# Kernel tuning notes

Hardware: AMD Instinct MI355X
Metric: run time of the kernel (lower is better)

Reference implementation:

```python
import jax, jax.numpy as jnp
from jax import lax
import numpy as np

DIM = 768        # d_model (mamba-130m)
D_IN = 1024      # vision encoder feature dim
NQ = 384         # num_queries
NB = 12          # num_blocks
BATCH = 2
LSEQ = 1024      # image tokens
DI = 2 * DIM     # mamba d_inner (expand=2)
DS = 16          # d_state
DC = 4           # d_conv
DTR = 48         # dt_rank = ceil(768/16)
NH = 16          # attention heads
HD = DIM // NH
NM = NB + 2      # mamba instances: fwd-enc, bwd-enc, one per block


def _ln(x, g, b):
    m = jnp.mean(x, -1, keepdims=True)
    v = jnp.mean((x - m) ** 2, -1, keepdims=True)
    return (x - m) * lax.rsqrt(v + 1e-5) * g + b


def _mamba(x, in_w, conv_w, conv_b, xproj_w, dt_w, dt_b, A_log, Dp, out_w):
    # x: (B, L, DIM)
    Bb = x.shape[0]
    xz = x @ in_w.T                      # (B, L, 2*DI)
    xi, z = jnp.split(xz, 2, -1)
    # depthwise causal conv1d over time
    xc = lax.conv_general_dilated(xi.transpose(0, 2, 1), conv_w[:, None, :], (1,),
                                  [(DC - 1, 0)], feature_group_count=DI,
                                  dimension_numbers=('NCH', 'OIH', 'NCH'))
    xc = jax.nn.silu((xc + conv_b[None, :, None]).transpose(0, 2, 1))  # (B, L, DI)
    dbl = xc @ xproj_w.T                 # (B, L, DTR + 2*DS)
    dt, Bm, Cm = jnp.split(dbl, [DTR, DTR + DS], -1)
    dt = jax.nn.softplus(dt @ dt_w.T + dt_b)   # (B, L, DI)
    A = -jnp.exp(A_log)                        # (DI, DS)
    dA = jnp.exp(dt[..., None] * A)            # (B, L, DI, DS)
    dBx = dt[..., None] * Bm[:, :, None, :] * xc[..., None]

    def step(h, inp):
        dA_t, dBx_t, C_t = inp
        h = dA_t * h + dBx_t
        return h, jnp.einsum('bds,bs->bd', h, C_t)

    h0 = jnp.zeros((Bb, DI, DS), x.dtype)
    _, ys = lax.scan(step, h0, (dA.transpose(1, 0, 2, 3), dBx.transpose(1, 0, 2, 3), Cm.transpose(1, 0, 2)))
    y = ys.transpose(1, 0, 2) + Dp * xc
    y = y * jax.nn.silu(z)
    return y @ out_w.T


def _local_allowed(nq, nk):
    # matches Attention.get_local_mask: query i attends to its contiguous key block
    kpq, extra = nk // nq, nk % nq
    i = jnp.arange(nq)
    start = i * kpq + jnp.minimum(i, extra)
    end = start + kpq + (i < extra)
    k = jnp.arange(nk)
    return (k[None, :] >= start[:, None]) & (k[None, :] < end[:, None])


def _mha(q_in, kv, in_w, in_b, out_w, out_b, allowed):
    # nn.MultiheadAttention(dim, 16, batch_first=True) cross-attention
    wq, wk, wv = jnp.split(in_w, 3, 0)
    bq, bk, bv = jnp.split(in_b, 3, 0)
    Bb = q_in.shape[0]
    q = (q_in @ wq.T + bq).reshape(Bb, -1, NH, HD)
    k = (kv @ wk.T + bk).reshape(Bb, -1, NH, HD)
    v = (kv @ wv.T + bv).reshape(Bb, -1, NH, HD)
    s = jnp.einsum('bqhd,bkhd->bhqk', q, k) / np.float32(np.sqrt(HD))
    s = jnp.where(allowed[None, None], s, -jnp.inf)
    a = jax.nn.softmax(s, -1)
    o = jnp.einsum('bhqk,bkhd->bqhd', a, v).reshape(Bb, -1, DIM)
    return o @ out_w.T + out_b


def _model(img_emb, queries, vision_proj_w, vision_proj_b, ln_vision_g, ln_vision_b,
           mamba_in_w, mamba_conv_w, mamba_conv_b, mamba_xproj_w, mamba_dt_w, mamba_dt_b,
           mamba_A_log, mamba_D, mamba_out_w, seq_norm_g, seq_norm_b,
           attn_in_w, attn_in_b, attn_out_w, attn_out_b, cross_w, cross_b):
    mp = lambda i: (mamba_in_w[i], mamba_conv_w[i], mamba_conv_b[i], mamba_xproj_w[i],
                    mamba_dt_w[i], mamba_dt_b[i], mamba_A_log[i], mamba_D[i], mamba_out_w[i])
    feats = _ln(img_emb @ vision_proj_w.T + vision_proj_b, ln_vision_g, ln_vision_b)
    fwd = _mamba(feats, *mp(0))
    bwd = jnp.flip(_mamba(jnp.flip(feats, 1), *mp(1)), 1)
    c = fwd + bwd + feats
    x = jnp.broadcast_to(queries, (img_emb.shape[0], NQ, DIM))
    allowed = _local_allowed(NQ, c.shape[1])
    for l in range(NB):
        x = _ln(x, seq_norm_g[l], seq_norm_b[l])
        x = _mamba(x, *mp(l + 2)) + x
        score = _mha(x, c, attn_in_w[l], attn_in_b[l], attn_out_w[l], attn_out_b[l], allowed)
        x = jnp.concatenate([x, score], -1) @ cross_w[l].T + cross_b[l]
    return x


_model_jit = jax.jit(_model)


def setup_inputs() -> dict:
    key = jax.random.key(0)
    ks = iter(jax.random.split(key, 24))
    rn = lambda shape, s=0.02: jax.random.normal(next(ks), shape, jnp.float32) * s
    A_log = jnp.broadcast_to(jnp.log(jnp.arange(1, DS + 1, dtype=jnp.float32)), (NM, DI, DS))
    return {
        'img_emb': rn((BATCH, LSEQ, D_IN), 1.0),
        'queries': rn((1, NQ, DIM)),
        'vision_proj_w': rn((DIM, D_IN)),
        'vision_proj_b': jnp.zeros((DIM,), jnp.float32),
        'ln_vision_g': jnp.ones((DIM,), jnp.float32),
        'ln_vision_b': jnp.zeros((DIM,), jnp.float32),
        'mamba_in_w': rn((NM, 2 * DI, DIM)),
        'mamba_conv_w': rn((NM, DI, DC), 0.1),
        'mamba_conv_b': jnp.zeros((NM, DI), jnp.float32),
        'mamba_xproj_w': rn((NM, DTR + 2 * DS, DI)),
        'mamba_dt_w': rn((NM, DI, DTR), 0.1),
        'mamba_dt_b': rn((NM, DI), 0.5),
        'mamba_A_log': A_log,
        'mamba_D': jnp.ones((NM, DI), jnp.float32),
        'mamba_out_w': rn((NM, DIM, DI)),
        'seq_norm_g': jnp.ones((NB, DIM), jnp.float32),
        'seq_norm_b': jnp.zeros((NB, DIM), jnp.float32),
        'attn_in_w': rn((NB, 3 * DIM, DIM)),
        'attn_in_b': jnp.zeros((NB, 3 * DIM), jnp.float32),
        'attn_out_w': rn((NB, DIM, DIM)),
        'attn_out_b': jnp.zeros((NB, DIM), jnp.float32),
        'cross_w': rn((NB, DIM, 2 * DIM)),
        'cross_b': jnp.zeros((NB, DIM), jnp.float32),
    }


def reference(img_emb, queries, vision_proj_w, vision_proj_b, ln_vision_g, ln_vision_b,
              mamba_in_w, mamba_conv_w, mamba_conv_b, mamba_xproj_w, mamba_dt_w, mamba_dt_b,
              mamba_A_log, mamba_D, mamba_out_w, seq_norm_g, seq_norm_b,
              attn_in_w, attn_in_b, attn_out_w, attn_out_b, cross_w, cross_b):
    return _model_jit(img_emb, queries, vision_proj_w, vision_proj_b, ln_vision_g, ln_vision_b,
                      mamba_in_w, mamba_conv_w, mamba_conv_b, mamba_xproj_w, mamba_dt_w, mamba_dt_b,
                      mamba_A_log, mamba_D, mamba_out_w, seq_norm_g, seq_norm_b,
                      attn_in_w, attn_in_b, attn_out_w, attn_out_b, cross_w, cross_b)
```

## Files before the change

kernel.cpp:

```cpp
#include <hip/hip_runtime.h>
#include <hip/hip_bf16.h>

#define DIMQ 768
#define D_IN 1024
#define NQ 384
#define NBK 12
#define BATCH 2
#define LSEQ 1024
#define DI 1536
#define DS 16
#define DTR 48
#define NH 16
#define HD 48

typedef __attribute__((ext_vector_type(8))) short short8;
typedef __attribute__((ext_vector_type(4))) float f32x4;

#define GF_BIAS 1
#define GF_SOFTPLUS 2
#define EPI_BIAS 1
#define EPI_ADDT 2

#define LOG2E 1.4426950408889634f

__device__ __forceinline__ unsigned short f2bf(float f) {
    unsigned int u = __builtin_bit_cast(unsigned int, f);
    u = (u + 0x7FFFu + ((u >> 16) & 1u)) >> 16;
    return (unsigned short)u;
}
__device__ __forceinline__ float bf2f(unsigned short h) {
    unsigned int u = ((unsigned int)h) << 16;
    return __builtin_bit_cast(float, u);
}

__device__ __forceinline__ void gload_lds16(const void* g, void* l) {
    __builtin_amdgcn_global_load_lds(
        (const __attribute__((address_space(1))) void*)g,
        (__attribute__((address_space(3))) void*)l, 16, 0, 0);
}

struct WTab {
    const float* src[10];
    long long dstOff[10];
    long long ps[10];
    int cum[10];
    int rows[10], cols[10], dcols[10];
    int n;
    int total;
};

__global__ void wconv_kernel(unsigned short* __restrict__ dst, WTab T)
{
    const int i = blockIdx.x * 256 + threadIdx.x;
    if (i >= T.total) return;
    int sI = 0;
    while (i >= T.cum[sI]) ++sI;
    const int e = i - (sI ? T.cum[sI - 1] : 0);
    const int dcols = T.dcols[sI];
    const int r = e / dcols;
    const int c = e - r * dcols;
    float v = 0.f;
    if (r < T.rows[sI] && c < T.cols[sI]) v = T.src[sI][(long long)r * T.cols[sI] + c];
    const unsigned short h = f2bf(v);
    const unsigned short l = f2bf(v - bf2f(h));
    dst[T.dstOff[sI] + e] = h;
    dst[T.dstOff[sI] + T.ps[sI] + e] = l;
}

struct LTab {
    const float* src[7];
    long long srcStride[7], dstOff[7], ps[7];
    int rows[7], cols[7], dcols[7], cum[7];
};

__global__ __launch_bounds__(256)
void wconv_layers(unsigned short* __restrict__ dst, long long layerStride, int lBase, LTab T)
{
    const int e = blockIdx.x * 256 + threadIdx.x;
    const int l = blockIdx.y + lBase;
    int sI = 0;
    while (e >= T.cum[sI]) ++sI;
    const int eo = e - (sI ? T.cum[sI - 1] : 0);
    const int dc = T.dcols[sI];
    const int r = eo / dc;
    const int c = eo - r * dc;
    float v = 0.f;
    if (r < T.rows[sI] && c < T.cols[sI])
        v = T.src[sI][(long long)l * T.srcStride[sI] + (long long)r * T.cols[sI] + c];
    const unsigned short h = f2bf(v);
    const unsigned short lo2 = f2bf(v - bf2f(h));
    unsigned short* d = dst + (long long)blockIdx.y * layerStride + T.dstOff[sI];
    d[eo] = h;
    d[T.ps[sI] + eo] = lo2;
}

__global__ __launch_bounds__(256, 3)
void gemm_direct(const float* __restrict__ Ag, const unsigned short* __restrict__ Bhl,
                 float* __restrict__ Cg, const float* __restrict__ biasg,
                 int M, int N, int K, int lda, int ldb, int ldc,
                 long long sA, long long sB, long long sC, long long sBias,
                 long long planeB, int flags)
{
    __shared__ __align__(16) unsigned short As[2][2][64][32];
    __shared__ __align__(16) unsigned short Bs[2][2][128][32];

    const int z = blockIdx.z;
    const float* A = Ag + (size_t)z * sA;
    const unsigned short* Bhi = Bhl + (size_t)z * sB;
    const unsigned short* Blo = Bhi + planeB;
    float* C = Cg + (size_t)z * sC;

    const int mBase = blockIdx.x * 64;
    const int nBase = blockIdx.y * 128;
    const int tid = threadIdx.x, lane = tid & 63, wave = tid >> 6;
    const int lm = lane & 15, lq = lane >> 4;
    const int wn = wave * 32;
    const int arow = tid >> 2, aq = tid & 3;
    const int brow = lane >> 2;
    const int bcol = ((lane & 3) ^ ((lane >> 3) & 3)) * 8;
    const int aunit = (aq ^ ((arow >> 1) & 3)) * 8;
    const int funit = (lq ^ ((lm >> 1) & 3)) * 8;

    const int ktiles = (K + 31) >> 5;

    auto issueB = [&](int t, int buf) {
#pragma unroll
        for (int cc = 0; cc < 4; ++cc) {
            const int chunk = wave * 4 + cc;
            const int pl = chunk >> 3;
            const int r16 = chunk & 7;
            const unsigned short* bp = pl ? Blo : Bhi;
            const int n = nBase + r16 * 16 + brow;
            gload_lds16(bp + (size_t)n * ldb + t * 32 + bcol, &Bs[buf][pl][r16 * 16][0]);
        }
    };
    auto loadA = [&](int t, float* v) {
        const int col = t * 32 + aq * 8;
        const float* src = A + (size_t)(mBase + arow) * lda + col;
#pragma unroll
        for (int u = 0; u < 2; ++u) {
            float4 t4 = make_float4(0.f, 0.f, 0.f, 0.f);
            if (col + u * 4 < K) t4 = *(const float4*)(src + u * 4);
            v[u*4+0]=t4.x; v[u*4+1]=t4.y; v[u*4+2]=t4.z; v[u*4+3]=t4.w;
        }
    };
    auto writeA = [&](const float* v, int buf) {
        short8 ph, plv;
#pragma unroll
        for (int j = 0; j < 8; ++j) {
            unsigned short h = f2bf(v[j]);
            ph[j] = (short)h;
            plv[j] = (short)f2bf(v[j] - bf2f(h));
        }
        *(short8*)&As[buf][0][arow][aunit] = ph;
        *(short8*)&As[buf][1][arow][aunit] = plv;
    };

    float av[8];
    issueB(0, 0);
    loadA(0, av);
    writeA(av, 0);

    f32x4 acc[4][2] = {};
    for (int t = 0; t < ktiles; ++t) {
        const int buf = t & 1;
        __syncthreads();
        const bool more = (t + 1) < ktiles;
        if (more) { issueB(t + 1, buf ^ 1); loadA(t + 1, av); }
        short8 ah[4], al[4], bh[2], bl[2];
#pragma unroll
        for (int i = 0; i < 4; ++i) {
            ah[i] = *(const short8*)&As[buf][0][16*i + lm][funit];
            al[i] = *(const short8*)&As[buf][1][16*i + lm][funit];
        }
#pragma unroll
        for (int j = 0; j < 2; ++j) {
            bh[j] = *(const short8*)&Bs[buf][0][wn + 16*j + lm][funit];
            bl[j] = *(const short8*)&Bs[buf][1][wn + 16*j + lm][funit];
        }
#pragma unroll
        for (int i = 0; i < 4; ++i)
#pragma unroll
            for (int j = 0; j < 2; ++j) {
                acc[i][j] = __builtin_amdgcn_mfma_f32_16x16x32_bf16(ah[i], bh[j], acc[i][j], 0, 0, 0);
                acc[i][j] = __builtin_amdgcn_mfma_f32_16x16x32_bf16(ah[i], bl[j], acc[i][j], 0, 0, 0);
                acc[i][j] = __builtin_amdgcn_mfma_f32_16x16x32_bf16(al[i], bh[j], acc[i][j], 0, 0, 0);
            }
        if (more) writeA(av, buf ^ 1);
    }

#pragma unroll
    for (int i = 0; i < 4; ++i)
#pragma unroll
        for (int j = 0; j < 2; ++j)
#pragma unroll
            for (int r = 0; r < 4; ++r) {
                const int m = mBase + i*16 + lq*4 + r;
                const int n = nBase + wn + j*16 + lm;
                float v = acc[i][j][r];
                if (flags & GF_BIAS)     v += biasg[(size_t)z * sBias + n];
                if (flags & GF_SOFTPLUS) v = (v > 20.f) ? v : log1pf(expf(v));
                C[(size_t)m * ldc + n] = v;
            }
}

__global__ __launch_bounds__(256, 3)
void gemm_splitk(const float* __restrict__ Ag, const unsigned short* __restrict__ Bhl,
                 float* __restrict__ Cp,
                 int M, int kLen, int S, int lda, int ldb, int ldP,
                 long long sA, long long sB, long long planeB)
{
    __shared__ __align__(16) unsigned short As[2][2][64][32];
    __shared__ __align__(16) unsigned short Bs[2][2][128][32];

    const int bz = blockIdx.z;
    const int s = bz % S, z = bz / S;
    const int kOff = s * kLen;
    const float* A = Ag + (size_t)z * sA;
    const unsigned short* Bhi = Bhl + (size_t)z * sB;
    const unsigned short* Blo = Bhi + planeB;

    const int mBase = blockIdx.x * 64;
    const int nBase = blockIdx.y * 128;
    const int tid = threadIdx.x, lane = tid & 63, wave = tid >> 6;
    const int lm = lane & 15, lq = lane >> 4;
    const int wn = wave * 32;
    const int arow = tid >> 2, aq = tid & 3;
    const int brow = lane >> 2;
    const int bcol = ((lane & 3) ^ ((lane >> 3) & 3)) * 8;
    const int aunit = (aq ^ ((arow >> 1) & 3)) * 8;
    const int funit = (lq ^ ((lm >> 1) & 3)) * 8;

    const int ktiles = kLen >> 5;

    auto issueB = [&](int t, int buf) {
#pragma unroll
        for (int cc = 0; cc < 4; ++cc) {
            const int chunk = wave * 4 + cc;
            const int pl = chunk >> 3;
            const int r16 = chunk & 7;
            const unsigned short* bp = pl ? Blo : Bhi;
            const int n = nBase + r16 * 16 + brow;
            gload_lds16(bp + (size_t)n * ldb + kOff + t * 32 + bcol, &Bs[buf][pl][r16 * 16][0]);
        }
    };
    auto loadA = [&](int t, float* v) {
        const float* src = A + (size_t)(mBase + arow) * lda + kOff + t * 32 + aq * 8;
#pragma unroll
        for (int u = 0; u < 2; ++u) {
            const float4 t4 = *(const float4*)(src + u * 4);
            v[u*4+0]=t4.x; v[u*4+1]=t4.y; v[u*4+2]=t4.z; v[u*4+3]=t4.w;
        }
    };
    auto writeA = [&](const float* v, int buf) {
        short8 ph, plv;
#pragma unroll
        for (int j = 0; j < 8; ++j) {
            unsigned short h = f2bf(v[j]);
            ph[j] = (short)h;
            plv[j] = (short)f2bf(v[j] - bf2f(h));
        }
        *(short8*)&As[buf][0][arow][aunit] = ph;
        *(short8*)&As[buf][1][arow][aunit] = plv;
    };

    float av[8];
    issueB(0, 0);
    loadA(0, av);
    writeA(av, 0);

    f32x4 acc[4][2] = {};
    for (int t = 0; t < ktiles; ++t) {
        const int buf = t & 1;
        __syncthreads();
        const bool more = (t + 1) < ktiles;
        if (more) { issueB(t + 1, buf ^ 1); loadA(t + 1, av); }
        short8 ah[4], al[4], bh[2], bl[2];
#pragma unroll
        for (int i = 0; i < 4; ++i) {
            ah[i] = *(const short8*)&As[buf][0][16*i + lm][funit];
            al[i] = *(const short8*)&As[buf][1][16*i + lm][funit];
        }
#pragma unroll
        for (int j = 0; j < 2; ++j) {
            bh[j] = *(const short8*)&Bs[buf][0][wn + 16*j + lm][funit];
            bl[j] = *(const short8*)&Bs[buf][1][wn + 16*j + lm][funit];
        }
#pragma unroll
        for (int i = 0; i < 4; ++i)
#pragma unroll
            for (int j = 0; j < 2; ++j) {
                acc[i][j] = __builtin_amdgcn_mfma_f32_16x16x32_bf16(ah[i], bh[j], acc[i][j], 0, 0, 0);
                acc[i][j] = __builtin_amdgcn_mfma_f32_16x16x32_bf16(ah[i], bl[j], acc[i][j], 0, 0, 0);
                acc[i][j] = __builtin_amdgcn_mfma_f32_16x16x32_bf16(al[i], bh[j], acc[i][j], 0, 0, 0);
            }
        if (more) writeA(av, buf ^ 1);
    }

    float* Cb = Cp + (size_t)bz * M * ldP;
#pragma unroll
    for (int i = 0; i < 4; ++i)
#pragma unroll
        for (int j = 0; j < 2; ++j)
#pragma unroll
            for (int r = 0; r < 4; ++r) {
                const int m = mBase + i*16 + lq*4 + r;
                const int n = nBase + wn + j*16 + lm;
                Cb[(size_t)m * ldP + n] = acc[i][j][r];
            }
}

__global__ void epi_kernel(const float* __restrict__ Cp, float* __restrict__ outF,
                           const float* __restrict__ bias, const float* __restrict__ addT,
                           int Z, int S, int M, int N, int ldP, int ldOut,
                           long long sOutZ, long long sBiasZ, int ldAdd, int flags)
{
    const int n4 = N >> 2;
    const int idx = blockIdx.x * 256 + threadIdx.x;
    if (idx >= Z * M * n4) return;
    const int c4 = idx % n4;
    const int rem = idx / n4;
    const int m = rem % M;
    const int z = rem / M;
    const int n = c4 * 4;
    const float* base = Cp + ((size_t)z * S * M + m) * ldP + n;
    float4 v = *(const float4*)base;
    for (int s = 1; s < S; ++s) {
        const float4 u = *(const float4*)(base + (size_t)s * M * ldP);
        v.x += u.x; v.y += u.y; v.z += u.z; v.w += u.w;
    }
    if (flags & EPI_BIAS) {
        const float4 b4 = *(const float4*)(bias + (size_t)z * sBiasZ + n);
        v.x += b4.x; v.y += b4.y; v.z += b4.z; v.w += b4.w;
    }
    if (flags & EPI_ADDT) {
        const float4 a4 = *(const float4*)(addT + (size_t)m * ldAdd + n);
        v.x += a4.x; v.y += a4.y; v.z += a4.z; v.w += a4.w;
    }
    *(float4*)(outF + (size_t)z * sOutZ + (size_t)m * ldOut + n) = v;
}

__global__ __launch_bounds__(256)
void epi_ln_kernel(const float* __restrict__ Cp, float* __restrict__ outF,
                   const float* __restrict__ bias,
                   const float* __restrict__ g, const float* __restrict__ b,
                   int S, int M, int ldP)
{
    const int m = blockIdx.x;
    const int tid = threadIdx.x;
    __shared__ float red[8];
    float v[3];
    float s = 0.f, s2 = 0.f;
#pragma unroll
    for (int j = 0; j < 3; ++j) {
        const int n = tid + j * 256;
        const float* pp = Cp + (size_t)m * ldP + n;
        float x = pp[0];
        for (int q = 1; q < S; ++q) x += pp[(size_t)q * M * ldP];
        x += bias[n];
        v[j] = x; s += x; s2 += x * x;
    }
#pragma unroll
    for (int o = 32; o; o >>= 1) { s += __shfl_xor(s, o); s2 += __shfl_xor(s2, o); }
    const int wv = tid >> 6;
    if ((tid & 63) == 0) { red[wv] = s; red[4 + wv] = s2; }
    __syncthreads();
    s  = red[0] + red[1] + red[2] + red[3];
    s2 = red[4] + red[5] + red[6] + red[7];
    const float mean = s * (1.f/768.f);
    const float var  = s2 * (1.f/768.f) - mean * mean;
    const float inv  = rsqrtf(var + 1e-5f);
#pragma unroll
    for (int j = 0; j < 3; ++j) {
        const int n = tid + j * 256;
        outF[(size_t)m * DIMQ + n] = (v[j] - mean) * inv * g[n] + b[n];
    }
}

__global__ void ln_kernel(const float* __restrict__ in, float* __restrict__ out,
                          const float* __restrict__ g, const float* __restrict__ b,
                          int rows, int srcMod)
{
    const int row = blockIdx.x * 4 + (threadIdx.x >> 6);
    const int lane = threadIdx.x & 63;
    if (row >= rows) return;
    const float* p = in + (size_t)(row % srcMod) * DIMQ;
    float v[12], s = 0.f, s2 = 0.f;
#pragma unroll
    for (int j = 0; j < 12; ++j) {
        v[j] = p[j*64 + lane];
        s += v[j];
        s2 += v[j]*v[j];
    }
#pragma unroll
    for (int o = 32; o; o >>= 1) { s += __shfl_xor(s, o); s2 += __shfl_xor(s2, o); }
    const float mean = s * (1.f/768.f);
    const float var  = s2 * (1.f/768.f) - mean*mean;
    const float inv  = rsqrtf(var + 1e-5f);
    float* q = out + (size_t)row * DIMQ;
#pragma unroll
    for (int j = 0; j < 12; ++j) {
        const int c = j*64 + lane;
        q[c] = (v[j] - mean) * inv * g[c] + b[c];
    }
}

__global__ void conv_kernel(const float* __restrict__ xz, float* __restrict__ xc,
                            const float* __restrict__ cw, const float* __restrict__ cb,
                            int Bn, int L, int instShift)
{
    const int idx = blockIdx.x * 256 + threadIdx.x;
    const int total = Bn * L * (DI/4);
    if (idx >= total) return;
    const int d4 = idx % (DI/4);
    const int t  = (idx / (DI/4)) % L;
    const int b  = idx / (L * (DI/4));
    const int inst = b >> instShift;
    const int d = d4 * 4;
    const float* base = xz + (size_t)(b * L) * 3072 + d;
    const float4 w0 = *(const float4*)(cw + (size_t)(inst*DI + d + 0) * 4);
    const float4 w1 = *(const float4*)(cw + (size_t)(inst*DI + d + 1) * 4);
    const float4 w2 = *(const float4*)(cw + (size_t)(inst*DI + d + 2) * 4);
    const float4 w3 = *(const float4*)(cw + (size_t)(inst*DI + d + 3) * 4);
    float4 acc = *(const float4*)(cb + (size_t)inst*DI + d);
    float4 xv[4];
#pragma unroll
    for (int j = 0; j < 4; ++j) {
        const int tt = t - 3 + j;
        xv[j] = (tt >= 0) ? *(const float4*)(base + (size_t)tt * 3072) : make_float4(0,0,0,0);
    }
    acc.x += xv[0].x*w0.x + xv[1].x*w0.y + xv[2].x*w0.z + xv[3].x*w0.w;
    acc.y += xv[0].y*w1.x + xv[1].y*w1.y + xv[2].y*w1.z + xv[3].y*w1.w;
    acc.z += xv[0].z*w2.x + xv[1].z*w2.y + xv[2].z*w2.z + xv[3].z*w2.w;
    acc.w += xv[0].w*w3.x + xv[1].w*w3.y + xv[2].w*w3.z + xv[3].w*w3.w;
    float4 o;
    o.x = acc.x / (1.f + expf(-acc.x));
    o.y = acc.y / (1.f + expf(-acc.y));
    o.z = acc.z / (1.f + expf(-acc.z));
    o.w = acc.w / (1.f + expf(-acc.w));
    *(float4*)(xc + (size_t)(b * L + t) * DI + d) = o;
}

__global__ __launch_bounds__(256)
void scan_p1(const float* __restrict__ dt, const float* __restrict__ dbl,
             const float* __restrict__ xc, const float* __restrict__ A_log,
             float* __restrict__ hend, float* __restrict__ sumdt,
             int L, int CL, int Bn, int instShift)
{
    const int d = blockIdx.x * 256 + threadIdx.x;
    const int b = blockIdx.y;
    const int c = blockIdx.z;
    const int inst = b >> instShift;
    const float* ap = A_log + ((size_t)inst * DI + d) * DS;
    float A2[16];
#pragma unroll
    for (int s = 0; s < 16; ++s) A2[s] = -expf(ap[s]) * LOG2E;
    float h[16] = {};
    float sd = 0.f;
    const int t0 = c * CL;
    const size_t rowbase = (size_t)b * L;
    for (int t = t0; t < t0 + CL; ++t) {
        const size_t row = rowbase + t;
        const float dtv = dt[row * DI + d];
        const float xcv = xc[row * DI + d];
        float Bv[16];
        *(float4*)(Bv + 0)  = *(const float4*)(dbl + row * 80 + 48);
        *(float4*)(Bv + 4)  = *(const float4*)(dbl + row * 80 + 52);
        *(float4*)(Bv + 8)  = *(const float4*)(dbl + row * 80 + 56);
        *(float4*)(Bv + 12) = *(const float4*)(dbl + row * 80 + 60);
        sd += dtv;
        const float bx = dtv * xcv;
#pragma unroll
        for (int s = 0; s < 16; ++s)
            h[s] = exp2f(dtv * A2[s]) * h[s] + bx * Bv[s];
    }
    float* hp = hend + (((size_t)c * Bn + b) * DI + d) * DS;
#pragma unroll
    for (int s = 0; s < 16; s += 4)
        *(float4*)(hp + s) = make_float4(h[s], h[s+1], h[s+2], h[s+3]);
    sumdt[((size_t)c * Bn + b) * DI + d] = sd;
}

__global__ void scan_p2(const float* __restrict__ hend, const float* __restrict__ sumdt,
                        const float* __restrict__ A_log, float* __restrict__ hstart,
                        int NC, int Bn, int instShift)
{
    const int gid = blockIdx.x * 256 + threadIdx.x;
    const int s = gid & 15;
    const int rem = gid >> 4;
    const int d = rem % DI;
    const int b = rem / DI;
    const int inst = b >> instShift;
    const float A2 = -expf(A_log[((size_t)inst * DI + d) * DS + s]) * LOG2E;
    float carry = 0.f;
    for (int c = 0; c < NC; ++c) {
        const size_t off = (((size_t)c * Bn + b) * DI + d) * DS + s;
        hstart[off] = carry;
        carry = exp2f(A2 * sumdt[((size_t)c * Bn + b) * DI + d]) * carry + hend[off];
    }
}

__global__ __launch_bounds__(256)
void scan_p3(const float* __restrict__ dt, const float* __restrict__ dbl,
             const float* __restrict__ xc, const float* __restrict__ xz,
             const float* __restrict__ A_log, const float* __restrict__ Dp,
             const float* __restrict__ hstart, float* __restrict__ y,
             int L, int CL, int Bn, int instShift)
{
    const int d = blockIdx.x * 256 + threadIdx.x;
    const int b = blockIdx.y;
    const int c = blockIdx.z;
    const int inst = b >> instShift;
    const float* ap = A_log + ((size_t)inst * DI + d) * DS;
    float A2[16];
#pragma unroll
    for (int s = 0; s < 16; ++s) A2[s] = -expf(ap[s]) * LOG2E;
    const float Dd = Dp[(size_t)inst * DI + d];
    float h[16];
    const float* hp = hstart + (((size_t)c * Bn + b) * DI + d) * DS;
#pragma unroll
    for (int s = 0; s < 16; s += 4) {
        const float4 t4 = *(const float4*)(hp + s);
        h[s] = t4.x; h[s+1] = t4.y; h[s+2] = t4.z; h[s+3] = t4.w;
    }
    const int t0 = c * CL;
    const size_t rowbase = (size_t)b * L;
    for (int t = t0; t < t0 + CL; ++t) {
        const size_t row = rowbase + t;
        const float dtv = dt[row * DI + d];
        const float xcv = xc[row * DI + d];
        const float zv  = xz[row * 3072 + DI + d];
        float Bv[16], Cv[16];
        *(float4*)(Bv + 0)  = *(const float4*)(dbl + row * 80 + 48);
        *(float4*)(Bv + 4)  = *(const float4*)(dbl + row * 80 + 52);
        *(float4*)(Bv + 8)  = *(const float4*)(dbl + row * 80 + 56);
        *(float4*)(Bv + 12) = *(const float4*)(dbl + row * 80 + 60);
        *(float4*)(Cv + 0)  = *(const float4*)(dbl + row * 80 + 64);
        *(float4*)(Cv + 4)  = *(const float4*)(dbl + row * 80 + 68);
        *(float4*)(Cv + 8)  = *(const float4*)(dbl + row * 80 + 72);
        *(float4*)(Cv + 12) = *(const float4*)(dbl + row * 80 + 76);
        const float bx = dtv * xcv;
#pragma unroll
        for (int s = 0; s < 16; ++s)
            h[s] = exp2f(dtv * A2[s]) * h[s] + bx * Bv[s];
        float p0 = 0.f, p1 = 0.f, p2 = 0.f, p3 = 0.f;
#pragma unroll
        for (int s = 0; s < 4; ++s) {
            p0 += h[s]      * Cv[s];
            p1 += h[s + 4]  * Cv[s + 4];
            p2 += h[s + 8]  * Cv[s + 8];
            p3 += h[s + 12] * Cv[s + 12];
        }
        const float p = (p0 + p1) + (p2 + p3);
        y[row * DI + d] = (p + Dd * xcv) * (zv / (1.f + expf(-zv)));
    }
}

__global__ void attn_kernel(const float* __restrict__ qP, const float* __restrict__ qBias,
                            const float* __restrict__ kv, float* __restrict__ o,
                            int S, int ldP)
{
    const int bi = blockIdx.x;
    const int b = bi / NQ, i = bi % NQ;
    const int tid = threadIdx.x;
    const int h = tid >> 2, r = tid & 3;
    int start, len;
    if (i < 256) { start = 3*i; len = 3; } else { start = 2*i + 256; len = 2; }
    const int col0 = h*48 + r*12;
    float qv[12];
#pragma unroll
    for (int u = 0; u < 12; ++u) {
        const int n = col0 + u;
        float x = qP[(size_t)bi * ldP + n];
        for (int s = 1; s < S; ++s) x += qP[((size_t)s * 768 + bi) * ldP + n];
        qv[u] = x + qBias[n];
    }
    float s[3] = {-1e30f, -1e30f, -1e30f};
    for (int j = 0; j < len; ++j) {
        const float* kp = kv + (size_t)(b*LSEQ + start + j) * 1536 + col0;
        float p = 0.f;
#pragma unroll
        for (int u = 0; u < 12; ++u) p += qv[u] * kp[u];
        p += __shfl_xor(p, 1);
        p += __shfl_xor(p, 2);
        s[j] = p * 0.14433756729740644f;
    }
    const float mx = fmaxf(s[0], fmaxf(s[1], s[2]));
    float e[3];
    e[0] = expf(s[0]-mx); e[1] = expf(s[1]-mx); e[2] = expf(s[2]-mx);
    const float inv = 1.f / (e[0] + e[1] + e[2]);
    float ov[12] = {};
    for (int j = 0; j < len; ++j) {
        const float w = e[j] * inv;
        const float* vp = kv + (size_t)(b*LSEQ + start + j) * 1536 + 768 + col0;
#pragma unroll
        for (int u = 0; u < 12; ++u) ov[u] += w * vp[u];
    }
    float* op = o + (size_t)bi * DIMQ + col0;
#pragma unroll
    for (int u = 0; u < 12; ++u) op[u] = ov[u];
}

__global__ void flip_kernel(float* __restrict__ X2)
{
    const int idx = blockIdx.x * 256 + threadIdx.x;
    if (idx >= 2*1024*192) return;
    const int d4 = idx % 192;
    const int t  = (idx / 192) % 1024;
    const int b  = idx / (192 * 1024);
    const size_t dst = ((size_t)((2+b)*1024 + t)) * DIMQ + d4*4;
    const size_t src = ((size_t)(b*1024 + (1023 - t))) * DIMQ + d4*4;
    *(float4*)(X2 + dst) = *(const float4*)(X2 + src);
}

__global__ void combine_kernel(const float* __restrict__ oe, const float* __restrict__ feats,
                               float* __restrict__ c)
{
    const int idx = blockIdx.x * 256 + threadIdx.x;
    if (idx >= 2*1024*192) return;
    const int d4 = idx % 192;
    const int t  = (idx / 192) % 1024;
    const int b  = idx / (192 * 1024);
    const size_t fw = ((size_t)(b*1024 + t)) * DIMQ + d4*4;
    const size_t bw = ((size_t)((2+b)*1024 + (1023 - t))) * DIMQ + d4*4;
    const float4 a = *(const float4*)(oe + fw);
    const float4 bb = *(const float4*)(oe + bw);
    const float4 f = *(const float4*)(feats + fw);
    float4 o;
    o.x = a.x + bb.x + f.x; o.y = a.y + bb.y + f.y;
    o.z = a.z + bb.z + f.z; o.w = a.w + bb.w + f.w;
    *(float4*)(c + fw) = o;
}

extern "C" void kernel_launch(void* const* d_in, const int* in_sizes, int n_in,
                              void* d_out, int out_size, void* d_ws, size_t ws_size,
                              hipStream_t stream) {
    const float* img_emb  = (const float*)d_in[0];
    const float* queries  = (const float*)d_in[1];
    const float* vis_w    = (const float*)d_in[2];
    const float* vis_b    = (const float*)d_in[3];
    const float* lnv_g    = (const float*)d_in[4];
    const float* lnv_b    = (const float*)d_in[5];
    const float* m_in_w   = (const float*)d_in[6];
    const float* m_conv_w = (const float*)d_in[7];
    const float* m_conv_b = (const float*)d_in[8];
    const float* m_xp_w   = (const float*)d_in[9];
    const float* m_dt_w   = (const float*)d_in[10];
    const float* m_dt_b   = (const float*)d_in[11];
    const float* m_A_log  = (const float*)d_in[12];
    const float* m_D      = (const float*)d_in[13];
    const float* m_out_w  = (const float*)d_in[14];
    const float* sn_g     = (const float*)d_in[15];
    const float* sn_b     = (const float*)d_in[16];
    const float* a_in_w   = (const float*)d_in[17];
    const float* a_in_b   = (const float*)d_in[18];
    const float* a_out_w  = (const float*)d_in[19];
    const float* a_out_b  = (const float*)d_in[20];
    const float* cr_w     = (const float*)d_in[21];
    const float* cr_b     = (const float*)d_in[22];
    float* out = (float*)d_out;

    float* ws = (float*)d_ws;
    auto alloc = [&](size_t n) { float* p = ws; ws += n; return p; };
    float* X2   = alloc((size_t)4096*768);
    float* xzb  = alloc((size_t)4096*3072);
    float* xcb  = alloc((size_t)4096*1536);
    float* dblb = alloc((size_t)4096*80);
    float* dtb  = alloc((size_t)4096*1536);
    float* yb   = alloc((size_t)4096*1536);
    float* oe   = alloc((size_t)4096*768);
    float* cbuf = alloc((size_t)2048*768);
    float* xn   = alloc((size_t)768*768);
    float* x1s  = alloc((size_t)768*1536);
    float* ob   = alloc((size_t)768*768);
    float* Cp   = alloc((size_t)2359296);
    unsigned short* wenc = (unsigned short*)alloc((size_t)16908288/2);

    const long long LAYER_USH = 14745600;
    const size_t usedFloats = (size_t)(ws - (float*)d_ws);
    const size_t needFull = (usedFloats + (size_t)12 * (LAYER_USH/2)) * 4;
    const bool bigW = ws_size >= needFull;
    unsigned short* wlayAll = (unsigned short*)ws;

    const size_t kvFloats = (size_t)12 * 2048 * 1536;
    const size_t needKV = needFull + kvFloats * 4;
    const bool kvHoist = bigW && ws_size >= needKV;
    float* kvAll = (float*)(wlayAll + (size_t)12 * LAYER_USH);

    const long long P_VIS = 768LL*1024;
    const long long P_IN  = 3072LL*768;
    const long long P_XP  = 128LL*1536;
    const long long P_DT  = 1536LL*64;
    const long long P_OUT = 768LL*1536;
    const long long P_AIN = 2304LL*768;
    const long long P_AOUT= 768LL*768;
    const long long P_CR  = 768LL*1536;
    const long long off_vis   = 0;
    const long long off_encIn = 2*P_VIS;
    const long long off_encXp = off_encIn + 4*P_IN;
    const long long off_encDt = off_encXp + 4*P_XP;
    const long long off_encOut= off_encDt + 4*P_DT;
    const long long off_in  = 0;
    const long long off_xp  = 2*P_IN;
    const long long off_dt  = off_xp + 2*P_XP;
    const long long off_out = off_dt + 2*P_DT;
    const long long off_aIn = off_out + 2*P_OUT;
    const long long off_aOut= off_aIn + 2*P_AIN;
    const long long off_cr  = off_aOut + 2*P_AOUT;

    auto addSeg = [](WTab& T, const float* src, int rows, int cols, int drows, int dcols,
                     long long dstOff) {
        const int k = T.n;
        T.src[k] = src; T.rows[k] = rows; T.cols[k] = cols; T.dcols[k] = dcols;
        T.ps[k] = (long long)drows * dcols;
        T.dstOff[k] = dstOff;
        T.total += drows * dcols;
        T.cum[k] = T.total;
        T.n = k + 1;
    };

    auto GD = [&](const float* A, const unsigned short* Bhl, long long planeB,
                  float* C, const float* bias,
                  int M, int N, int K, int lda, int ldb, int ldc,
                  long long sA, long long sB, long long sC, long long sBias,
                  int Z, int flags) {
        dim3 grid(M/64, N/128, Z);
        gemm_direct<<<grid, 256, 0, stream>>>(A, Bhl, C, bias, M, N, K, lda, ldb, ldc,
                                              sA, sB, sC, sBias, planeB, flags);
    };
    auto GS = [&](const float* A, const unsigned short* Bhl, long long planeB,
                  int M, int Ntile, int kLen, int S, int lda, int ldb, int ldP,
                  long long sA, long long sB, int Z) {
        dim3 grid(M/64, Ntile/128, Z*S);
        gemm_splitk<<<grid, 256, 0, stream>>>(A, Bhl, Cp, M, kLen, S, lda, ldb, ldP,
                                              sA, sB, planeB);
    };
    auto EPI = [&](float* outF, const float* bias, const float* addT,
                   int Z, int S, int M, int N, int ldP, int ldOut,
                   long long sOutZ, long long sBiasZ, int ldAdd, int flags) {
        const int total = Z * M * (N/4);
        epi_kernel<<<(total+255)/256, 256, 0, stream>>>(Cp, outF, bias, addT, Z, S, M, N,
                                                        ldP, ldOut, sOutZ, sBiasZ, ldAdd, flags);
    };

    {
        WTab T = {}; T.n = 0; T.total = 0;
        addSeg(T, vis_w, 768, 1024, 768, 1024, off_vis);
        addSeg(T, m_in_w,               3072, 768, 3072, 768, off_encIn);
        addSeg(T, m_in_w + 3072*768,    3072, 768, 3072, 768, off_encIn + 2*P_IN);
        addSeg(T, m_xp_w,               80, 1536, 128, 1536, off_encXp);
        addSeg(T, m_xp_w + 80*1536,     80, 1536, 128, 1536, off_encXp + 2*P_XP);
        addSeg(T, m_dt_w,               1536, 48, 1536, 64, off_encDt);
        addSeg(T, m_dt_w + 1536*48,     1536, 48, 1536, 64, off_encDt + 2*P_DT);
        addSeg(T, m_out_w,              768, 1536, 768, 1536, off_encOut);
        addSeg(T, m_out_w + 768*1536,   768, 1536, 768, 1536, off_encOut + 2*P_OUT);
        wconv_kernel<<<(T.total+255)/256, 256, 0, stream>>>(wenc, T);
    }

    LTab LT = {};
    {
        auto seg = [&](int k, const float* src, long long srcStride, int rows, int cols,
                       int drows, int dcols, long long dstOff) {
            LT.src[k] = src; LT.srcStride[k] = srcStride;
            LT.rows[k] = rows; LT.cols[k] = cols; LT.dcols[k] = dcols;
            LT.ps[k] = (long long)drows * dcols; LT.dstOff[k] = dstOff;
            LT.cum[k] = (k ? LT.cum[k-1] : 0) + drows * dcols;
        };
        seg(0, m_in_w  + (size_t)2*3072*768, 3072LL*768, 3072, 768, 3072, 768, off_in);
        seg(1, m_xp_w  + (size_t)2*80*1536,  80LL*1536,  80, 1536, 128, 1536, off_xp);
        seg(2, m_dt_w  + (size_t)2*1536*48,  1536LL*48,  1536, 48, 1536, 64, off_dt);
        seg(3, m_out_w + (size_t)2*768*1536, 768LL*1536, 768, 1536, 768, 1536, off_out);
        seg(4, a_in_w,  2304LL*768, 2304, 768, 2304, 768, off_aIn);
        seg(5, a_out_w, 768LL*768,  768, 768, 768, 768, off_aOut);
        seg(6, cr_w,    768LL*1536, 768, 1536, 768, 1536, off_cr);
    }
    if (bigW)
        wconv_layers<<<dim3(28800, 12), 256, 0, stream>>>(wlayAll, LAYER_USH, 0, LT);

    GD(img_emb, wenc + off_vis, P_VIS, oe, vis_b,
       2048, 768, 1024, 1024, 1024, 768, 0,0,0,0, 1, GF_BIAS);
    ln_kernel<<<512, 256, 0, stream>>>(oe, X2, lnv_g, lnv_b, 2048, 2048);
    flip_kernel<<<(2*1024*192 + 255)/256, 256, 0, stream>>>(X2);

    GD(X2, wenc + off_encIn, P_IN, xzb, nullptr,
       2048, 3072, 768, 768, 768, 3072, 2048LL*768, 2*P_IN, 2048LL*3072, 0, 2, 0);
    conv_kernel<<<(4*1024*384 + 255)/256, 256, 0, stream>>>(xzb, xcb, m_conv_w, m_conv_b, 4, 1024, 1);
    GS(xcb, wenc + off_encXp, P_XP, 2048, 128, 384, 4, 1536, 1536, 128,
       2048LL*1536, 2*P_XP, 2);
    EPI(dblb, nullptr, nullptr, 2, 4, 2048, 80, 128, 80, 2048LL*80, 0, 0, 0);
    GD(dblb, wenc + off_encDt, P_DT, dtb, m_dt_b,
       2048, 1536, 48, 80, 64, 1536, 2048LL*80, 2*P_DT, 2048LL*1536, 1536, 2,
       GF_BIAS | GF_SOFTPLUS);
    {
        const int NC = 16, CL = 64;
        float* hend   = oe;
        float* hstart = oe + (size_t)NC*4*DI*DS;
        float* sumdt  = cbuf;
        scan_p1<<<dim3(6, 4, NC), 256, 0, stream>>>(dtb, dblb, xcb, m_A_log, hend, sumdt, 1024, CL, 4, 1);
        scan_p2<<<(4*DI*DS)/256, 256, 0, stream>>>(hend, sumdt, m_A_log, hstart, NC, 4, 1);
        scan_p3<<<dim3(6, 4, NC), 256, 0, stream>>>(dtb, dblb, xcb, xzb, m_A_log, m_D, hstart, yb, 1024, CL, 4, 1);
    }
    GD(yb, wenc + off_encOut, P_OUT, oe, nullptr,
       2048, 768, 1536, 1536, 1536, 768, 2048LL*1536, 2*P_OUT, 2048LL*768, 0, 2, 0);
    combine_kernel<<<(2*1024*192 + 255)/256, 256, 0, stream>>>(oe, X2, cbuf);

    if (kvHoist)
        GD(cbuf, wlayAll + off_aIn + 768LL*768, P_AIN, kvAll, a_in_b + 768,
           2048, 1536, 768, 768, 768, 1536,
           0, LAYER_USH, 2048LL*1536, 2304, 12, GF_BIAS);

    ln_kernel<<<192, 256, 0, stream>>>(queries, xn, sn_g, sn_b, 768, 384);

    for (int l = 0; l < NBK; ++l) {
        const int li = l + 2;
        const unsigned short* wl = bigW ? wlayAll + (size_t)l * LAYER_USH : wlayAll;
        if (!bigW)
            wconv_layers<<<dim3(28800, 1), 256, 0, stream>>>((unsigned short*)wlayAll, LAYER_USH, l, LT);

        GD(xn, wl + off_in, P_IN, xzb, nullptr,
           768, 3072, 768, 768, 768, 3072, 0,0,0,0, 1, 0);
        conv_kernel<<<(2*NQ*384 + 255)/256, 256, 0, stream>>>(
            xzb, xcb, m_conv_w + (size_t)li*DI*4, m_conv_b + (size_t)li*DI, 2, NQ, 8);
        GS(xcb, wl + off_xp, P_XP, 768, 128, 96, 16, 1536, 1536, 128, 0, 0, 1);
        EPI(dblb, nullptr, nullptr, 1, 16, 768, 80, 128, 80, 0, 0, 0, 0);
        GD(dblb, wl + off_dt, P_DT, dtb, m_dt_b + (size_t)li*1536,
           768, 1536, 48, 80, 64, 1536, 0,0,0,0, 1, GF_BIAS | GF_SOFTPLUS);
        {
            const int NC = 24, CL = 16;
            const float* Ap = m_A_log + (size_t)li*DI*DS;
            float* hend   = oe;
            float* hstart = oe + (size_t)NC*2*DI*DS;
            float* sumdt  = oe + (size_t)2*NC*2*DI*DS;
            scan_p1<<<dim3(6, 2, NC), 256, 0, stream>>>(dtb, dblb, xcb, Ap, hend, sumdt, NQ, CL, 2, 8);
            scan_p2<<<(2*DI*DS)/256, 256, 0, stream>>>(hend, sumdt, Ap, hstart, NC, 2, 8);
            scan_p3<<<dim3(6, 2, NC), 256, 0, stream>>>(dtb, dblb, xcb, xzb, Ap, m_D + (size_t)li*DI,
                                                        hstart, yb, NQ, CL, 2, 8);
        }
        GS(yb, wl + off_out, P_OUT, 768, 768, 384, 4, 1536, 1536, 768, 0, 0, 1);
        EPI(x1s, nullptr, xn, 1, 4, 768, 768, 768, 1536, 0, 0, 768, EPI_ADDT);
        GS(x1s, wl + off_aIn, P_AIN, 768, 768, 192, 4, 1536, 768, 768, 0, 0, 1);
        const float* kvp;
        if (kvHoist) {
            kvp = kvAll + (size_t)l * 2048 * 1536;
        } else {
            GD(cbuf, wl + off_aIn + 768LL*768, P_AIN, oe, a_in_b + (size_t)l*2304 + 768,
               2048, 1536, 768, 768, 768, 1536, 0,0,0,0, 1, GF_BIAS);
            kvp = oe;
        }
        attn_kernel<<<2*NQ, 64, 0, stream>>>(Cp, a_in_b + (size_t)l*2304, kvp, ob, 4, 768);
        GS(ob, wl + off_aOut, P_AOUT, 768, 768, 192, 4, 768, 768, 768, 0, 0, 1);
        EPI(x1s + 768, a_out_b + (size_t)l*768, nullptr, 1, 4, 768, 768, 768, 1536, 0, 0, 0, EPI_BIAS);
        GS(x1s, wl + off_cr, P_CR, 768, 768, 384, 4, 1536, 1536, 768, 0, 0, 1);
        if (l == NBK - 1) {
            EPI(out, cr_b + (size_t)l*768, nullptr, 1, 4, 768, 768, 768, 768, 0, 0, 0, EPI_BIAS);
        } else {
            epi_ln_kernel<<<768, 256, 0, stream>>>(Cp, xn, cr_b + (size_t)l*768,
                                                   sn_g + (size_t)(l+1)*768,
                                                   sn_b + (size_t)(l+1)*768,
                                                   4, 768, 768);
        }
    }
}
```

Before: 4.131 ms.

## Add 128x128 GEMM tile kernel, in-place scan carry, and finer scan chunking

Adds a 512-thread GEMM variant with 128x128 output tiles using split-bf16 MFMA and uses it for the large encoder in-projection and KV projections. The goal is more A/B reuse per block and fewer blocks than the 64x128 tile. The scan's second pass now rewrites chunk-end states in place as chunk-start states, which drops a separate buffer. Chunk counts are doubled for the encoder and per-block scans to expose more parallelism. The trade-off is more pass-2 sequential steps and higher register and LDS pressure per block in the new GEMM.

Measured after the change: 4.381 ms. 6.0% more time.

```diff
diff --git a/kernel.cpp b/kernel.cpp
--- a/kernel.cpp
+++ b/kernel.cpp
@@ -204,6 +204,117 @@
             }
 }
 
+__global__ __launch_bounds__(512)
+void gemm_direct128(const float* __restrict__ Ag, const unsigned short* __restrict__ Bhl,
+                    float* __restrict__ Cg, const float* __restrict__ biasg,
+                    int M, int N, int K, int lda, int ldb, int ldc,
+                    long long sA, long long sB, long long sC, long long sBias,
+                    long long planeB, int flags)
+{
+    __shared__ __align__(16) unsigned short As[2][2][128][32];
+    __shared__ __align__(16) unsigned short Bs[2][2][128][32];
+
+    const int z = blockIdx.z;
+    const float* A = Ag + (size_t)z * sA;
+    const unsigned short* Bhi = Bhl + (size_t)z * sB;
+    const unsigned short* Blo = Bhi + planeB;
+    float* C = Cg + (size_t)z * sC;
+
+    const int mBase = blockIdx.x * 128;
+    const int nBase = blockIdx.y * 128;
+    const int tid = threadIdx.x, lane = tid & 63, wave = tid >> 6;
+    const int lm = lane & 15, lq = lane >> 4;
+    const int wr = (wave >> 2) * 64;
+    const int wc = (wave & 3) * 32;
+    const int arow = tid >> 2, aq = tid & 3;
+    const int brow = lane >> 2;
+    const int bcol = ((lane & 3) ^ ((lane >> 3) & 3)) * 8;
+    const int aunit = (aq ^ ((arow >> 1) & 3)) * 8;
+    const int funit = (lq ^ ((lm >> 1) & 3)) * 8;
+
+    const int ktiles = (K + 31) >> 5;
+
+    auto issueB = [&](int t, int buf) {
+#pragma unroll
+        for (int cc = 0; cc < 2; ++cc) {
+            const int chunk = wave * 2 + cc;
+            const int pl = chunk >> 3;
+            const int r16 = chunk & 7;
+            const unsigned short* bp = pl ? Blo : Bhi;
+            const int n = nBase + r16 * 16 + brow;
+            gload_lds16(bp + (size_t)n * ldb + t * 32 + bcol, &Bs[buf][pl][r16 * 16][0]);
+        }
+    };
+    auto loadA = [&](int t, float* v) {
+        const int col = t * 32 + aq * 8;
+        const float* src = A + (size_t)(mBase + arow) * lda + col;
+#pragma unroll
+        for (int u = 0; u < 2; ++u) {
+            float4 t4 = make_float4(0.f, 0.f, 0.f, 0.f);
+            if (col + u * 4 < K) t4 = *(const float4*)(src + u * 4);
+            v[u*4+0]=t4.x; v[u*4+1]=t4.y; v[u*4+2]=t4.z; v[u*4+3]=t4.w;
+        }
+    };
+    auto writeA = [&](const float* v, int buf) {
+        short8 ph, plv;
+#pragma unroll
+        for (int j = 0; j < 8; ++j) {
+            unsigned short h = f2bf(v[j]);
+            ph[j] = (short)h;
+            plv[j] = (short)f2bf(v[j] - bf2f(h));
+        }
+        *(short8*)&As[buf][0][arow][aunit] = ph;
+        *(short8*)&As[buf][1][arow][aunit] = plv;
+    };
+
+    float av[8];
+    issueB(0, 0);
+    loadA(0, av);
+    writeA(av, 0);
+
+    f32x4 acc[4][2] = {};
+    for (int t = 0; t < ktiles; ++t) {
+        const int buf = t & 1;
+        __syncthreads();
+        const bool more = (t + 1) < ktiles;
+        if (more) { issueB(t + 1, buf ^ 1); loadA(t + 1, av); }
+        short8 ah[4], al[4], bh[2], bl[2];
+#pragma unroll
+        for (int i = 0; i < 4; ++i) {
+            ah[i] = *(const short8*)&As[buf][0][wr + 16*i + lm][funit];
+            al[i] = *(const short8*)&As[buf][1][wr + 16*i + lm][funit];
+        }
+#pragma unroll
+        for (int j = 0; j < 2; ++j) {
+            bh[j] = *(const short8*)&Bs[buf][0][wc + 16*j + lm][funit];
+            bl[j] = *(const short8*)&Bs[buf][1][wc + 16*j + lm][funit];
+        }
+#pragma unroll
+        for (int i = 0; i < 4; ++i)
+#pragma unroll
+            for (int j = 0; j < 2; ++j) {
+                acc[i][j] = __builtin_amdgcn_mfma_f32_16x16x32_bf16(ah[i], bh[j], acc[i][j], 0, 0, 0);
+                acc[i][j] = __builtin_amdgcn_mfma_f32_16x16x32_bf16(ah[i], bl[j], acc[i][j], 0, 0, 0);
+                acc[i][j] = __builtin_amdgcn_mfma_f32_16x16x32_bf16(al[i], bh[j], acc[i][j], 0, 0, 0);
+            }
+        if (more) writeA(av, buf ^ 1);
+    }
+
+#pragma unroll
+    for (int i = 0; i < 4; ++i)
+#pragma unroll
+        for (int j = 0; j < 2; ++j)
+#pragma unroll
+            for (int r = 0; r < 4; ++r) {
+                const int m = mBase + wr + i*16 + lq*4 + r;
+                const int n = nBase + wc + j*16 + lm;
+                float v = acc[i][j][r];
+                if (flags & GF_BIAS)     v += biasg[(size_t)z * sBias + n];
+                if (flags & GF_SOFTPLUS) v = (v > 20.f) ? v : log1pf(expf(v));
+                C[(size_t)m * ldc + n] = v;
+            }
+}
+
 __global__ __launch_bounds__(256, 3)
 void gemm_splitk(const float* __restrict__ Ag, const unsigned short* __restrict__ Bhl,
                  float* __restrict__ Cp,
@@ -481,9 +592,9 @@
     sumdt[((size_t)c * Bn + b) * DI + d] = sd;
 }
 
-__global__ void scan_p2(const float* __restrict__ hend, const float* __restrict__ sumdt,
-                        const float* __restrict__ A_log, float* __restrict__ hstart,
-                        int NC, int Bn, int instShift)
+__global__ void scan_p2ip(float* hbuf, const float* __restrict__ sumdt,
+                          const float* __restrict__ A_log,
+                          int NC, int Bn, int instShift)
 {
     const int gid = blockIdx.x * 256 + threadIdx.x;
     const int s = gid & 15;
@@ -495,8 +606,9 @@
     float carry = 0.f;
     for (int c = 0; c < NC; ++c) {
         const size_t off = (((size_t)c * Bn + b) * DI + d) * DS + s;
-        hstart[off] = carry;
-        carry = exp2f(A2 * sumdt[((size_t)c * Bn + b) * DI + d]) * carry + hend[off];
+        const float he = hbuf[off];
+        hbuf[off] = carry;
+        carry = exp2f(A2 * sumdt[((size_t)c * Bn + b) * DI + d]) * carry + he;
     }
 }
 
@@ -728,6 +840,15 @@
         gemm_direct<<<grid, 256, 0, stream>>>(A, Bhl, C, bias, M, N, K, lda, ldb, ldc,
                                               sA, sB, sC, sBias, planeB, flags);
     };
+    auto GD128 = [&](const float* A, const unsigned short* Bhl, long long planeB,
+                     float* C, const float* bias,
+                     int M, int N, int K, int lda, int ldb, int ldc,
+                     long long sA, long long sB, long long sC, long long sBias,
+                     int Z, int flags) {
+        dim3 grid(M/128, N/128, Z);
+        gemm_direct128<<<grid, 512, 0, stream>>>(A, Bhl, C, bias, M, N, K, lda, ldb, ldc,
+                                                 sA, sB, sC, sBias, planeB, flags);
+    };
     auto GS = [&](const float* A, const unsigned short* Bhl, long long planeB,
                   int M, int Ntile, int kLen, int S, int lda, int ldb, int ldP,
                   long long sA, long long sB, int Z) {
@@ -782,8 +903,8 @@
     ln_kernel<<<512, 256, 0, stream>>>(oe, X2, lnv_g, lnv_b, 2048, 2048);
     flip_kernel<<<(2*1024*192 + 255)/256, 256, 0, stream>>>(X2);
 
-    GD(X2, wenc + off_encIn, P_IN, xzb, nullptr,
-       2048, 3072, 768, 768, 768, 3072, 2048LL*768, 2*P_IN, 2048LL*3072, 0, 2, 0);
+    GD128(X2, wenc + off_encIn, P_IN, xzb, nullptr,
+          2048, 3072, 768, 768, 768, 3072, 2048LL*768, 2*P_IN, 2048LL*3072, 0, 2, 0);
     conv_kernel<<<(4*1024*384 + 255)/256, 256, 0, stream>>>(xzb, xcb, m_conv_w, m_conv_b, 4, 1024, 1);
     GS(xcb, wenc + off_encXp, P_XP, 2048, 128, 384, 4, 1536, 1536, 128,
        2048LL*1536, 2*P_XP, 2);
@@ -792,22 +913,21 @@
        2048, 1536, 48, 80, 64, 1536, 2048LL*80, 2*P_DT, 2048LL*1536, 1536, 2,
        GF_BIAS | GF_SOFTPLUS);
     {
-        const int NC = 16, CL = 64;
+        const int NC = 32, CL = 32;
         float* hend   = oe;
-        float* hstart = oe + (size_t)NC*4*DI*DS;
         float* sumdt  = cbuf;
         scan_p1<<<dim3(6, 4, NC), 256, 0, stream>>>(dtb, dblb, xcb, m_A_log, hend, sumdt, 1024, CL, 4, 1);
-        scan_p2<<<(4*DI*DS)/256, 256, 0, stream>>>(hend, sumdt, m_A_log, hstart, NC, 4, 1);
-        scan_p3<<<dim3(6, 4, NC), 256, 0, stream>>>(dtb, dblb, xcb, xzb, m_A_log, m_D, hstart, yb, 1024, CL, 4, 1);
+        scan_p2ip<<<(4*DI*DS)/256, 256, 0, stream>>>(hend, sumdt, m_A_log, NC, 4, 1);
+        scan_p3<<<dim3(6, 4, NC), 256, 0, stream>>>(dtb, dblb, xcb, xzb, m_A_log, m_D, hend, yb, 1024, CL, 4, 1);
     }
     GD(yb, wenc + off_encOut, P_OUT, oe, nullptr,
        2048, 768, 1536, 1536, 1536, 768, 2048LL*1536, 2*P_OUT, 2048LL*768, 0, 2, 0);
     combine_kernel<<<(2*1024*192 + 255)/256, 256, 0, stream>>>(oe, X2, cbuf);
 
     if (kvHoist)
-        GD(cbuf, wlayAll + off_aIn + 768LL*768, P_AIN, kvAll, a_in_b + 768,
-           2048, 1536, 768, 768, 768, 1536,
-           0, LAYER_USH, 2048LL*1536, 2304, 12, GF_BIAS);
+        GD128(cbuf, wlayAll + off_aIn + 768LL*768, P_AIN, kvAll, a_in_b + 768,
+              2048, 1536, 768, 768, 768, 1536,
+              0, LAYER_USH, 2048LL*1536, 2304, 12, GF_BIAS);
 
     ln_kernel<<<192, 256, 0, stream>>>(queries, xn, sn_g, sn_b, 768, 384);
 
@@ -826,15 +946,14 @@
         GD(dblb, wl + off_dt, P_DT, dtb, m_dt_b + (size_t)li*1536,
            768, 1536, 48, 80, 64, 1536, 0,0,0,0, 1, GF_BIAS | GF_SOFTPLUS);
         {
-            const int NC = 24, CL = 16;
+            const int NC = 48, CL = 8;
             const float* Ap = m_A_log + (size_t)li*DI*DS;
             float* hend   = oe;
-            float* hstart = oe + (size_t)NC*2*DI*DS;
-            float* sumdt  = oe + (size_t)2*NC*2*DI*DS;
+            float* sumdt  = oe + (size_t)NC*2*DI*DS;
             scan_p1<<<dim3(6, 2, NC), 256, 0, stream>>>(dtb, dblb, xcb, Ap, hend, sumdt, NQ, CL, 2, 8);
-            scan_p2<<<(2*DI*DS)/256, 256, 0, stream>>>(hend, sumdt, Ap, hstart, NC, 2, 8);
+            scan_p2ip<<<(2*DI*DS)/256, 256, 0, stream>>>(hend, sumdt, Ap, NC, 2, 8);
             scan_p3<<<dim3(6, 2, NC), 256, 0, stream>>>(dtb, dblb, xcb, xzb, Ap, m_D + (size_t)li*DI,
-                                                        hstart, yb, NQ, CL, 2, 8);
+                                                        hend, yb, NQ, CL, 2, 8);
         }
         GS(yb, wl + off_out, P_OUT, 768, 768, 384, 4, 1536, 1536, 768, 0, 0, 1);
         EPI(x1s, nullptr, xn, 1, 4, 768, 768, 768, 1536, 0, 0, 768, EPI_ADDT);
@@ -843,8 +962,8 @@
         if (kvHoist) {
             kvp = kvAll + (size_t)l * 2048 * 1536;
         } else {
-            GD(cbuf, wl + off_aIn + 768LL*768, P_AIN, oe, a_in_b + (size_t)l*2304 + 768,
-               2048, 1536, 768, 768, 768, 1536, 0,0,0,0, 1, GF_BIAS);
+            GD128(cbuf, wl + off_aIn + 768LL*768, P_AIN, oe, a_in_b + (size_t)l*2304 + 768,
+                  2048, 1536, 768, 768, 768, 1536, 0,0,0,0, 1, GF_BIAS);
             kvp = oe;
         }
         attn_kernel<<<2*NQ, 64, 0, stream>>>(Cp, a_in_b + (size_t)l*2304, kvp, ob, 4, 768);
```
